# Performance work log

Measured on AMD Instinct MI355X. Metric: run time of the kernel, lower is better.

The kernel has to match this reference:

```python
import jax, jax.numpy as jnp
import numpy as np

B, N, D = 8, 1024, 768
H = 12
HD = D // H  # 64
SCALE = HD ** -0.5


def setup_inputs() -> dict:
    key = jax.random.key(0)
    k1, k2, k3 = jax.random.split(key, 3)
    x = jax.random.normal(k1, (B, N, D), dtype=jnp.float32)
    qkv_w = jax.random.normal(k2, (3 * D, D), dtype=jnp.float32) * 0.02
    proj_w = jax.random.normal(k3, (D, D), dtype=jnp.float32) * 0.02
    proj_b = jnp.zeros((D,), dtype=jnp.float32)
    return {"x": x, "qkv_w": qkv_w, "proj_w": proj_w, "proj_b": proj_b}


def reference(x, qkv_w, proj_w, proj_b):
    # qkv projection: [B,N,3D] -> [3,B,H,N,HD]
    qkv = jnp.einsum('bnd,ed->bne', x, qkv_w)
    qkv = qkv.reshape(B, N, 3, H, HD).transpose(2, 0, 3, 1, 4)
    q, k, v = qkv[0], qkv[1], qkv[2]
    # scaled dot-product attention
    attn = jnp.einsum('bhqd,bhkd->bhqk', q * SCALE, k)
    attn = jax.nn.softmax(attn, axis=-1)
    out = jnp.einsum('bhqk,bhkd->bhqd', attn, v)
    out = out.transpose(0, 2, 1, 3).reshape(B, N, D)
    # output projection
    return jnp.einsum('bnd,ed->bne', out, proj_w) + proj_b
```

## Files before the change

kernel.cpp:

```cpp
#include <hip/hip_runtime.h>

typedef unsigned short ushort;
typedef __attribute__((ext_vector_type(4)))  float  f32x4;
typedef __attribute__((ext_vector_type(16))) float  f32x16;
typedef __attribute__((ext_vector_type(8)))  short  s16x8;
typedef __attribute__((ext_vector_type(4)))  ushort u16x4;
typedef __attribute__((ext_vector_type(4)))  unsigned u32x4;

#define MFMA16(a, b, c) __builtin_amdgcn_mfma_f32_16x16x32_bf16((a), (b), (c), 0, 0, 0)
#define MFMA32(a, b, c) __builtin_amdgcn_mfma_f32_32x32x16_bf16((a), (b), (c), 0, 0, 0)

__device__ __forceinline__ ushort f2bf(float f) {
    unsigned u = __builtin_bit_cast(unsigned, f);
    u = (u + 0x7FFF + ((u >> 16) & 1)) >> 16;
    return (ushort)u;
}

__device__ __forceinline__ unsigned cvtpk_bf16(float lo, float hi) {
    unsigned r;
    asm("v_cvt_pk_bf16_f32 %0, %1, %2" : "=v"(r) : "v"(lo), "v"(hi));
    return r;
}
__device__ __forceinline__ void plswap(unsigned& a, unsigned& b) {
    asm volatile("v_permlane32_swap_b32 %0, %1" : "+v"(a), "+v"(b));
}
__device__ __forceinline__ float pairmax(float x) {
    unsigned a = __builtin_bit_cast(unsigned, x), b;
    asm("v_mov_b32 %0, %1" : "=v"(b) : "v"(a));
    plswap(a, b);
    return fmaxf(__builtin_bit_cast(float, a), __builtin_bit_cast(float, b));
}
__device__ __forceinline__ float pairsum(float x) {
    unsigned a = __builtin_bit_cast(unsigned, x), b;
    asm("v_mov_b32 %0, %1" : "=v"(b) : "v"(a));
    plswap(a, b);
    return __builtin_bit_cast(float, a) + __builtin_bit_cast(float, b);
}
__device__ __forceinline__ float fast_exp2(float x) {
    float r;
    asm("v_exp_f32 %0, %1" : "=v"(r) : "v"(x));
    return r;
}

__device__ __forceinline__ void gload_lds16(const ushort* g, ushort* l) {
    __builtin_amdgcn_global_load_lds(
        (const __attribute__((address_space(1))) void*)g,
        (__attribute__((address_space(3))) void*)l, 16, 0, 0);
}

__global__ __launch_bounds__(256) void cvt_all(
    const float* __restrict__ x, const float* __restrict__ wq,
    const float* __restrict__ wp, ushort* __restrict__ out,
    int n4x, int n4q, int n4p)
{
    int i = blockIdx.x * blockDim.x + threadIdx.x;
    const int stride = gridDim.x * blockDim.x;
    const int total = n4x + n4q + n4p;
    for (; i < total; i += stride) {
        float4 v;
        if (i < n4x)            v = ((const float4*)x)[i];
        else if (i < n4x + n4q) v = ((const float4*)wq)[i - n4x];
        else                    v = ((const float4*)wp)[i - n4x - n4q];
        u16x4 o;
        o[0] = f2bf(v.x); o[1] = f2bf(v.y); o[2] = f2bf(v.z); o[3] = f2bf(v.w);
        ((u16x4*)out)[i] = o;
    }
}

__device__ __forceinline__ void gemm128_mainloop(
    const ushort* __restrict__ A, const ushort* __restrict__ B, int K,
    int row0, int col0, ushort* As, ushort* Bs, f32x4 acc[4][4])
{
    const int t  = threadIdx.x;
    const int l  = t & 63;
    const int w  = t >> 6;
    const int lr = l & 15, lg = l >> 4;
    const int wm = w >> 1, wn = w & 1;

#pragma unroll
    for (int m = 0; m < 4; m++)
#pragma unroll
        for (int n = 0; n < 4; n++) acc[m][n] = (f32x4){0.f, 0.f, 0.f, 0.f};

    const int slot = (t & 3) ^ ((t >> 3) & 3);
    const ushort* ga0 = A + (row0 + (t >> 2)) * K + slot * 8;
    const ushort* gb0 = B + (col0 + (t >> 2)) * K + slot * 8;
    const int rowsz = 64 * K;
    ushort* la0 = As + t * 8;
    ushort* lb0 = Bs + t * 8;

    auto STAGE = [&](int kt, int buf) {
        const int k0  = kt * 32;
        const int off = buf * 4096;
        gload_lds16(ga0 + k0,         la0 + off);
        gload_lds16(ga0 + rowsz + k0, la0 + off + 2048);
        gload_lds16(gb0 + k0,         lb0 + off);
        gload_lds16(gb0 + rowsz + k0, lb0 + off + 2048);
    };
    const int sx = (lg ^ ((lr >> 1) & 3)) * 8;
    auto COMPUTE = [&](int buf) {
        const ushort* Ab = As + buf * 4096;
        const ushort* Bb = Bs + buf * 4096;
        s16x8 af[4], bfr[4];
#pragma unroll
        for (int m = 0; m < 4; m++)
            af[m] = *(const s16x8*)&Ab[(wm * 64 + m * 16 + lr) * 32 + sx];
#pragma unroll
        for (int n = 0; n < 4; n++)
            bfr[n] = *(const s16x8*)&Bb[(wn * 64 + n * 16 + lr) * 32 + sx];
        __builtin_amdgcn_s_setprio(1);
#pragma unroll
        for (int m = 0; m < 4; m++)
#pragma unroll
            for (int n = 0; n < 4; n++)
                acc[m][n] = MFMA16(af[m], bfr[n], acc[m][n]);
        __builtin_amdgcn_s_setprio(0);
    };

    const int nt = K >> 5;
    STAGE(0, 0);
    STAGE(1, 1);
    asm volatile("s_waitcnt vmcnt(4)" ::: "memory");
    __builtin_amdgcn_s_barrier();

#define GSTEP(IT, CBUF, SBUF)                                          \
    {                                                                  \
        const int sk = (IT) + 2;                                       \
        const bool st = sk < nt;                                       \
        if (st) STAGE(sk, SBUF);                                       \
        COMPUTE(CBUF);                                                 \
        if (st) { asm volatile("s_waitcnt vmcnt(4)" ::: "memory"); }   \
        else    { asm volatile("s_waitcnt vmcnt(0)" ::: "memory"); }   \
        __builtin_amdgcn_s_barrier();                                  \
    }

    for (int base = 0; base < nt; base += 3) {
        GSTEP(base,     0, 2);
        GSTEP(base + 1, 1, 0);
        GSTEP(base + 2, 2, 1);
    }
#undef GSTEP
}

__global__ __launch_bounds__(256) void qkv_gemm(
    const ushort* __restrict__ X, const ushort* __restrict__ W,
    ushort* __restrict__ qb, ushort* __restrict__ kb, ushort* __restrict__ vb)
{
    __shared__ __align__(16) ushort As[3 * 128 * 32];
    __shared__ __align__(16) ushort Bs[3 * 128 * 32];
    f32x4 acc[4][4];
    const int br = blockIdx.x, bc = blockIdx.y;
    gemm128_mainloop(X, W, 768, br * 128, bc * 128, As, Bs, acc);

    const int t = threadIdx.x, l = t & 63, w = t >> 6;
    const int lr = l & 15, lg = l >> 4, wm = w >> 1, wn = w & 1;
    const int p = (bc * 128) / 768;
    const int mrow0 = br * 128 + wm * 64 + lg * 4;
    const int ecolB = bc * 128 + wn * 64 + lr;
    const float QSCALE = 0.125f * 1.44269504088896f;

#pragma unroll
    for (int n = 0; n < 4; n++) {
        const int e   = ecolB + n * 16;
        const int rem = e - p * 768;
        const int h   = rem >> 6;
        const int hd  = rem & 63;
#pragma unroll
        for (int m = 0; m < 4; m++) {
            const int mr = mrow0 + m * 16;
            const int b  = mr >> 10;
            const int nn = mr & 1023;
            const f32x4 v = acc[m][n];
            const int bh = b * 12 + h;
            if (p == 0) {
                ushort* dst = qb + (bh * 1024 + nn) * 64 + hd;
#pragma unroll
                for (int r = 0; r < 4; r++) dst[r * 64] = f2bf(v[r] * QSCALE);
            } else if (p == 1) {
                ushort* dst = kb + (bh * 1024 + nn) * 64 + hd;
#pragma unroll
                for (int r = 0; r < 4; r++) dst[r * 64] = f2bf(v[r]);
            } else {
                u16x4 pk;
                pk[0] = f2bf(v[0]); pk[1] = f2bf(v[1]);
                pk[2] = f2bf(v[2]); pk[3] = f2bf(v[3]);
                *(u16x4*)(vb + (bh * 64 + hd) * 1024 + nn) = pk;
            }
        }
    }
}

__global__ __launch_bounds__(256) void attn_kernel(
    const ushort* __restrict__ qb, const ushort* __restrict__ kb,
    const ushort* __restrict__ vb, ushort* __restrict__ ao)
{
    __shared__ __align__(16) ushort KV[3][4096];
    const int bh = blockIdx.x, qt = blockIdx.y;
    const int b = bh / 12, h = bh - b * 12;
    const int t = threadIdx.x, l = t & 63, w = t >> 6;
    const int lq = l & 31, hi = l >> 5;
    const int qr0 = qt * 128 + w * 32;

    const int l3 = l >> 3, l7 = l & 7;
    const int ku = w * 8 + l3;
    const int pfv = l7 ^ l3;
    const char* ksrc = (const char*)kb + (size_t)(bh * 1024 + ku) * 128
                     + ((l7 ^ l3) << 4);
    const char* vsrc = (const char*)vb + (size_t)(bh * 64 + ku + 32 * ((pfv >> 2) & 1)) * 2048
                     + ((pfv & 3) << 4);
    ushort* kdst = &KV[0][0]    + t * 8;
    ushort* vdst = &KV[0][2048] + t * 8;

    auto STAGE = [&](int kt, int buf) {
        gload_lds16((const ushort*)(ksrc + kt * 32 * 128), kdst + buf * 4096);
        gload_lds16((const ushort*)(vsrc + kt * 32 * 2),   vdst + buf * 4096);
    };

    const ushort* qlane = qb + (bh * 1024 + qr0 + lq) * 64 + hi * 8;
    s16x8 qf[4];
#pragma unroll
    for (int s = 0; s < 4; s++) qf[s] = *(const s16x8*)(qlane + s * 16);

    float m = -__builtin_inff();
    float lsum = 0.f;
    f32x16 o0 = {}, o1 = {};

    STAGE(0, 0);
    STAGE(1, 1);
    asm volatile("s_waitcnt vmcnt(2)" ::: "memory");
    __builtin_amdgcn_s_barrier();

    const int fx = (lq & 7) << 4;
    int cur = 0;
    for (int it = 0; it < 32; ++it) {
        const bool st = it < 30;
        if (st) {
            int sb = cur + 2; if (sb >= 3) sb -= 3;
            STAGE(it + 2, sb);
        }
        const char* Kb = (const char*)&KV[cur][0];
        const char* Vb = (const char*)&KV[cur][2048];

        s16x8 kf[4];
#pragma unroll
        for (int s = 0; s < 4; s++)
            kf[s] = *(const s16x8*)(Kb + lq * 128 + ((hi * 16 + s * 32) ^ fx));

        f32x16 sa = {};
        __builtin_amdgcn_s_setprio(1);
#pragma unroll
        for (int s = 0; s < 4; s++) sa = MFMA32(kf[s], qf[s], sa);
        __builtin_amdgcn_s_setprio(0);

        float g0 = fmaxf(fmaxf(sa[0],  sa[1]),  sa[2]);
        float g1 = fmaxf(fmaxf(sa[3],  sa[4]),  sa[5]);
        float g2 = fmaxf(fmaxf(sa[6],  sa[7]),  sa[8]);
        float g3 = fmaxf(fmaxf(sa[9],  sa[10]), sa[11]);
        float g4 = fmaxf(fmaxf(sa[12], sa[13]), sa[14]);
        float h0 = fmaxf(fmaxf(g0, g1), g2);
        float h1 = fmaxf(fmaxf(g3, g4), sa[15]);
        const float mx = pairmax(fmaxf(h0, h1));

        if (!__all(mx <= m + 8.f)) {
            const float mn = fmaxf(m, mx);
            const float fac = fast_exp2(m - mn);
            m = mn;
            lsum *= fac;
#pragma unroll
            for (int r = 0; r < 16; r++) { o0[r] *= fac; o1[r] *= fac; }
        }

        float p[16];
#pragma unroll
        for (int r = 0; r < 16; r++) p[r] = fast_exp2(sa[r] - m);
        float ts[8];
#pragma unroll
        for (int r = 0; r < 8; r++) ts[r] = p[r] + p[r + 8];
#pragma unroll
        for (int s = 4; s; s >>= 1)
#pragma unroll
            for (int r = 0; r < s; r++) ts[r] += ts[r + s];
        lsum += pairsum(ts[0]);

        s16x8 pfr[2];
#pragma unroll
        for (int slot = 0; slot < 2; slot++) {
            const int r0 = slot * 8;
            unsigned a0 = cvtpk_bf16(p[r0 + 0], p[r0 + 1]);
            unsigned a1 = cvtpk_bf16(p[r0 + 4], p[r0 + 5]);
            plswap(a0, a1);
            unsigned b0 = cvtpk_bf16(p[r0 + 2], p[r0 + 3]);
            unsigned b1 = cvtpk_bf16(p[r0 + 6], p[r0 + 7]);
            plswap(b0, b1);
            const u32x4 u = {a0, b0, a1, b1};
            pfr[slot] = __builtin_bit_cast(s16x8, u);
        }

        s16x8 vf[2][2];
#pragma unroll
        for (int half = 0; half < 2; half++)
#pragma unroll
            for (int s = 0; s < 2; s++)
                vf[half][s] = *(const s16x8*)(Vb + lq * 128 + ((half * 64 + hi * 16 + s * 32) ^ fx));
        __builtin_amdgcn_s_setprio(1);
        o0 = MFMA32(vf[0][0], pfr[0], o0);
        o1 = MFMA32(vf[1][0], pfr[0], o1);
        o0 = MFMA32(vf[0][1], pfr[1], o0);
        o1 = MFMA32(vf[1][1], pfr[1], o1);
        __builtin_amdgcn_s_setprio(0);

        if (st) { asm volatile("s_waitcnt vmcnt(2)" ::: "memory"); }
        else    { asm volatile("s_waitcnt vmcnt(0)" ::: "memory"); }
        __builtin_amdgcn_s_barrier();
        cur = (cur == 2) ? 0 : cur + 1;
    }

    const float inv = 1.f / lsum;
    ushort* op = ao + (b * 1024 + qr0 + lq) * 768 + h * 64 + 4 * hi;
#pragma unroll
    for (int i = 0; i < 4; i++) {
        u16x4 pk0, pk1;
#pragma unroll
        for (int j = 0; j < 4; j++) {
            pk0[j] = f2bf(o0[4 * i + j] * inv);
            pk1[j] = f2bf(o1[4 * i + j] * inv);
        }
        *(u16x4*)(op + 8 * i)      = pk0;
        *(u16x4*)(op + 32 + 8 * i) = pk1;
    }
}

__global__ __launch_bounds__(256) void proj_gemm(
    const ushort* __restrict__ A, const ushort* __restrict__ W,
    const float* __restrict__ bias, float* __restrict__ out)
{
    __shared__ __align__(16) ushort As[3 * 64 * 32];
    __shared__ __align__(16) ushort Bs[3 * 128 * 32];
    const int t = threadIdx.x, l = t & 63, w = t >> 6;
    const int lr = l & 15, lg = l >> 4;
    const int wm = w >> 1, wn = w & 1;
    const int br = blockIdx.x, bc = blockIdx.y;

    f32x4 acc[2][4];
#pragma unroll
    for (int m = 0; m < 2; m++)
#pragma unroll
        for (int n = 0; n < 4; n++) acc[m][n] = (f32x4){0.f, 0.f, 0.f, 0.f};

    const int slot = (t & 3) ^ ((t >> 3) & 3);
    const ushort* ga0 = A + (br * 64 + (t >> 2)) * 768 + slot * 8;
    const ushort* gb0 = W + (bc * 128 + (t >> 2)) * 768 + slot * 8;
    ushort* la0 = As + t * 8;
    ushort* lb0 = Bs + t * 8;

    auto STAGE = [&](int kt, int buf) {
        const int k0 = kt * 32;
        gload_lds16(ga0 + k0,            la0 + buf * 2048);
        gload_lds16(gb0 + k0,            lb0 + buf * 4096);
        gload_lds16(gb0 + 64 * 768 + k0, lb0 + buf * 4096 + 2048);
    };
    const int sx = (lg ^ ((lr >> 1) & 3)) * 8;
    auto COMPUTE = [&](int buf) {
        const ushort* Ab = As + buf * 2048;
        const ushort* Bb = Bs + buf * 4096;
        s16x8 af[2], bfr[4];
#pragma unroll
        for (int m = 0; m < 2; m++)
            af[m] = *(const s16x8*)&Ab[(wm * 32 + m * 16 + lr) * 32 + sx];
#pragma unroll
        for (int n = 0; n < 4; n++)
            bfr[n] = *(const s16x8*)&Bb[(wn * 64 + n * 16 + lr) * 32 + sx];
        __builtin_amdgcn_s_setprio(1);
#pragma unroll
        for (int m = 0; m < 2; m++)
#pragma unroll
            for (int n = 0; n < 4; n++)
                acc[m][n] = MFMA16(af[m], bfr[n], acc[m][n]);
        __builtin_amdgcn_s_setprio(0);
    };

    const int nt = 24;
    STAGE(0, 0);
    STAGE(1, 1);
    asm volatile("s_waitcnt vmcnt(3)" ::: "memory");
    __builtin_amdgcn_s_barrier();

#define GSTEP(IT, CBUF, SBUF)                                          \
    {                                                                  \
        const int sk = (IT) + 2;                                       \
        const bool st = sk < nt;                                       \
        if (st) STAGE(sk, SBUF);                                       \
        COMPUTE(CBUF);                                                 \
        if (st) { asm volatile("s_waitcnt vmcnt(3)" ::: "memory"); }   \
        else    { asm volatile("s_waitcnt vmcnt(0)" ::: "memory"); }   \
        __builtin_amdgcn_s_barrier();                                  \
    }

    for (int base = 0; base < nt; base += 3) {
        GSTEP(base,     0, 2);
        GSTEP(base + 1, 1, 0);
        GSTEP(base + 2, 2, 1);
    }
#undef GSTEP

    const int mrow0 = br * 64 + wm * 32 + lg * 4;
    const int ecolB = bc * 128 + wn * 64 + lr;
#pragma unroll
    for (int n = 0; n < 4; n++) {
        const int e = ecolB + n * 16;
        const float bv = bias[e];
#pragma unroll
        for (int m = 0; m < 2; m++) {
            const int mr = mrow0 + m * 16;
#pragma unroll
            for (int r = 0; r < 4; r++)
                out[(mr + r) * 768 + e] = acc[m][n][r] + bv;
        }
    }
}

extern "C" void kernel_launch(void* const* d_in, const int* in_sizes, int n_in,
                              void* d_out, int out_size, void* d_ws, size_t ws_size,
                              hipStream_t stream)
{
    const float* x  = (const float*)d_in[0];
    const float* wq = (const float*)d_in[1];
    const float* wp = (const float*)d_in[2];
    const float* pb = (const float*)d_in[3];
    float* out = (float*)d_out;

    const int NX = 8 * 1024 * 768;
    const int NQ = 2304 * 768;
    const int NP = 768 * 768;
    const int SEG = 8 * 12 * 1024 * 64;

    ushort* xb  = (ushort*)d_ws;
    ushort* wqb = xb + NX;
    ushort* wpb = wqb + NQ;
    ushort* qb  = wpb + NP;
    ushort* kb  = qb + SEG;
    ushort* vb  = kb + SEG;
    ushort* ao  = xb;

    cvt_all<<<2048, 256, 0, stream>>>(x, wq, wp, xb, NX / 4, NQ / 4, NP / 4);

    qkv_gemm  <<<dim3(64, 18), 256, 0, stream>>>(xb, wqb, qb, kb, vb);
    attn_kernel<<<dim3(96, 8), 256, 0, stream>>>(qb, kb, vb, ao);
    proj_gemm <<<dim3(128, 6), 256, 0, stream>>>(ao, wpb, pb, out);
}
```

Measured before the change: 119.5 us.

## Split attention KV range across wave pairs and merge partial softmax states

Each attention block now handles 64 query rows instead of 128. Two waves share each 32-row strip, and each wave processes half of the key/value sequence, so the grid doubles to 96x16. The partial max, sum and output from the two halves are merged through LDS at the end. The staging changes from a 3-deep ring to double buffering, with __syncthreads in place of the finer vmcnt waits. The aim is more blocks and shorter serial loops per wave, at the cost of a merge step, a full barrier every iteration, and less prefetch depth.

```diff
diff --git a/kernel.cpp b/kernel.cpp
--- a/kernel.cpp
+++ b/kernel.cpp
@@ -194,26 +194,31 @@
     const ushort* __restrict__ qb, const ushort* __restrict__ kb,
     const ushort* __restrict__ vb, ushort* __restrict__ ao)
 {
-    __shared__ __align__(16) ushort KV[3][4096];
+    __shared__ __align__(16) ushort KV[2][8192];
     const int bh = blockIdx.x, qt = blockIdx.y;
     const int b = bh / 12, h = bh - b * 12;
     const int t = threadIdx.x, l = t & 63, w = t >> 6;
     const int lq = l & 31, hi = l >> 5;
-    const int qr0 = qt * 128 + w * 32;
-
-    const int l3 = l >> 3, l7 = l & 7;
-    const int ku = w * 8 + l3;
-    const int pfv = l7 ^ l3;
-    const char* ksrc = (const char*)kb + (size_t)(bh * 1024 + ku) * 128
-                     + ((l7 ^ l3) << 4);
-    const char* vsrc = (const char*)vb + (size_t)(bh * 64 + ku + 32 * ((pfv >> 2) & 1)) * 2048
+    const int strip = w & 1, half = w >> 1;
+    const int qr0 = qt * 64 + strip * 32;
+
+    const int u   = t >> 3;
+    const int pfv = (t & 7) ^ (u & 7);
+    const char* ksrc = (const char*)kb + (size_t)(bh * 1024 + u) * 128 + (pfv << 4);
+    const char* vsrc = (const char*)vb
+                     + (size_t)(bh * 64 + u + 32 * ((pfv >> 2) & 1)) * 2048
                      + ((pfv & 3) << 4);
-    ushort* kdst = &KV[0][0]    + t * 8;
-    ushort* vdst = &KV[0][2048] + t * 8;
+    ushort* kd0 = &KV[0][0]    + t * 8;
+    ushort* vd0 = &KV[0][2048] + t * 8;
+    ushort* kd1 = &KV[0][4096] + t * 8;
+    ushort* vd1 = &KV[0][6144] + t * 8;
 
     auto STAGE = [&](int kt, int buf) {
-        gload_lds16((const ushort*)(ksrc + kt * 32 * 128), kdst + buf * 4096);
-        gload_lds16((const ushort*)(vsrc + kt * 32 * 2),   vdst + buf * 4096);
+        const int bo = buf * 8192;
+        gload_lds16((const ushort*)(ksrc + kt * 4096),           kd0 + bo);
+        gload_lds16((const ushort*)(vsrc + kt * 64),             vd0 + bo);
+        gload_lds16((const ushort*)(ksrc + 65536 + kt * 4096),   kd1 + bo);
+        gload_lds16((const ushort*)(vsrc + 1024 + kt * 64),      vd1 + bo);
     };
 
     const ushort* qlane = qb + (bh * 1024 + qr0 + lq) * 64 + hi * 8;
@@ -226,20 +231,15 @@
     f32x16 o0 = {}, o1 = {};
 
     STAGE(0, 0);
-    STAGE(1, 1);
-    asm volatile("s_waitcnt vmcnt(2)" ::: "memory");
-    __builtin_amdgcn_s_barrier();
+    __syncthreads();
 
     const int fx = (lq & 7) << 4;
-    int cur = 0;
-    for (int it = 0; it < 32; ++it) {
-        const bool st = it < 30;
-        if (st) {
-            int sb = cur + 2; if (sb >= 3) sb -= 3;
-            STAGE(it + 2, sb);
-        }
-        const char* Kb = (const char*)&KV[cur][0];
-        const char* Vb = (const char*)&KV[cur][2048];
+    const int hoff = half * 8192;
+    for (int it = 0; it < 16; ++it) {
+        const int cur = it & 1;
+        if (it < 15) STAGE(it + 1, cur ^ 1);
+        const char* Kb = (const char*)&KV[cur][0] + hoff;
+        const char* Vb = Kb + 4096;
 
         s16x8 kf[4];
 #pragma unroll
@@ -292,16 +292,16 @@
             unsigned b0 = cvtpk_bf16(p[r0 + 2], p[r0 + 3]);
             unsigned b1 = cvtpk_bf16(p[r0 + 6], p[r0 + 7]);
             plswap(b0, b1);
-            const u32x4 u = {a0, b0, a1, b1};
-            pfr[slot] = __builtin_bit_cast(s16x8, u);
+            const u32x4 uu = {a0, b0, a1, b1};
+            pfr[slot] = __builtin_bit_cast(s16x8, uu);
         }
 
         s16x8 vf[2][2];
 #pragma unroll
-        for (int half = 0; half < 2; half++)
+        for (int hd = 0; hd < 2; hd++)
 #pragma unroll
             for (int s = 0; s < 2; s++)
-                vf[half][s] = *(const s16x8*)(Vb + lq * 128 + ((half * 64 + hi * 16 + s * 32) ^ fx));
+                vf[hd][s] = *(const s16x8*)(Vb + lq * 128 + ((hd * 64 + hi * 16 + s * 32) ^ fx));
         __builtin_amdgcn_s_setprio(1);
         o0 = MFMA32(vf[0][0], pfr[0], o0);
         o1 = MFMA32(vf[1][0], pfr[0], o1);
@@ -309,24 +309,45 @@
         o1 = MFMA32(vf[1][1], pfr[1], o1);
         __builtin_amdgcn_s_setprio(0);
 
-        if (st) { asm volatile("s_waitcnt vmcnt(2)" ::: "memory"); }
-        else    { asm volatile("s_waitcnt vmcnt(0)" ::: "memory"); }
-        __builtin_amdgcn_s_barrier();
-        cur = (cur == 2) ? 0 : cur + 1;
-    }
-
-    const float inv = 1.f / lsum;
-    ushort* op = ao + (b * 1024 + qr0 + lq) * 768 + h * 64 + 4 * hi;
-#pragma unroll
-    for (int i = 0; i < 4; i++) {
-        u16x4 pk0, pk1;
-#pragma unroll
-        for (int j = 0; j < 4; j++) {
-            pk0[j] = f2bf(o0[4 * i + j] * inv);
-            pk1[j] = f2bf(o1[4 * i + j] * inv);
-        }
-        *(u16x4*)(op + 8 * i)      = pk0;
-        *(u16x4*)(op + 32 + 8 * i) = pk1;
+        __syncthreads();
+    }
+
+    float* ex = (float*)&KV[0][0];
+    float* sb = ex + strip * 2176;
+    __syncthreads();
+    if (half == 1) {
+        sb[l] = m;
+        sb[64 + l] = lsum;
+#pragma unroll
+        for (int r = 0; r < 16; r++) sb[128  + r * 64 + l] = o0[r];
+#pragma unroll
+        for (int r = 0; r < 16; r++) sb[1152 + r * 64 + l] = o1[r];
+    }
+    __syncthreads();
+    if (half == 0) {
+        const float mb = sb[l], lb = sb[64 + l];
+        const float mm = fmaxf(m, mb);
+        const float fa = fast_exp2(m - mm);
+        const float fb = fast_exp2(mb - mm);
+        const float lt = lsum * fa + lb * fb;
+#pragma unroll
+        for (int r = 0; r < 16; r++) {
+            o0[r] = o0[r] * fa + sb[128  + r * 64 + l] * fb;
+            o1[r] = o1[r] * fa + sb[1152 + r * 64 + l] * fb;
+        }
+        const float inv = 1.f / lt;
+        ushort* op = ao + (b * 1024 + qr0 + lq) * 768 + h * 64 + 4 * hi;
+#pragma unroll
+        for (int i = 0; i < 4; i++) {
+            u16x4 pk0, pk1;
+#pragma unroll
+            for (int j = 0; j < 4; j++) {
+                pk0[j] = f2bf(o0[4 * i + j] * inv);
+                pk1[j] = f2bf(o1[4 * i + j] * inv);
+            }
+            *(u16x4*)(op + 8 * i)      = pk0;
+            *(u16x4*)(op + 32 + 8 * i) = pk1;
+        }
     }
 }
 
@@ -445,6 +466,6 @@
     cvt_all<<<2048, 256, 0, stream>>>(x, wq, wp, xb, NX / 4, NQ / 4, NP / 4);
 
     qkv_gemm  <<<dim3(64, 18), 256, 0, stream>>>(xb, wqb, qb, kb, vb);
-    attn_kernel<<<dim3(96, 8), 256, 0, stream>>>(qb, kb, vb, ao);
+    attn_kernel<<<dim3(96, 16), 256, 0, stream>>>(qb, kb, vb, ao);
     proj_gemm <<<dim3(128, 6), 256, 0, stream>>>(ao, wpb, pb, out);
 }
```

Result: no change. 120.5 us (+0.8%).

## Replace triple-buffered K/V LDS pipeline with double buffering

Applied to the files above, without the earlier changes.

The attention kernel's K/V staging goes from three LDS buffers with prefetch distance two to two buffers with prefetch distance one. The explicit vmcnt waits are replaced by __syncthreads. This cuts LDS use per block from 24 KB to 16 KB, which may allow more blocks per CU. In exchange, less global-load latency is hidden, and __syncthreads likely waits for all outstanding loads every iteration.

```diff
diff --git a/kernel.cpp b/kernel.cpp
--- a/kernel.cpp
+++ b/kernel.cpp
@@ -194,7 +194,7 @@
     const ushort* __restrict__ qb, const ushort* __restrict__ kb,
     const ushort* __restrict__ vb, ushort* __restrict__ ao)
 {
-    __shared__ __align__(16) ushort KV[3][4096];
+    __shared__ __align__(16) ushort KV[2][4096];
     const int bh = blockIdx.x, qt = blockIdx.y;
     const int b = bh / 12, h = bh - b * 12;
     const int t = threadIdx.x, l = t & 63, w = t >> 6;
@@ -208,13 +208,8 @@
                      + ((l7 ^ l3) << 4);
     const char* vsrc = (const char*)vb + (size_t)(bh * 64 + ku + 32 * ((pfv >> 2) & 1)) * 2048
                      + ((pfv & 3) << 4);
-    ushort* kdst = &KV[0][0]    + t * 8;
-    ushort* vdst = &KV[0][2048] + t * 8;
-
-    auto STAGE = [&](int kt, int buf) {
-        gload_lds16((const ushort*)(ksrc + kt * 32 * 128), kdst + buf * 4096);
-        gload_lds16((const ushort*)(vsrc + kt * 32 * 2),   vdst + buf * 4096);
-    };
+    ushort* kdst = &KV[0][0]    + w * 512 + l * 8;
+    ushort* vdst = &KV[0][2048] + w * 512 + l * 8;
 
     const ushort* qlane = qb + (bh * 1024 + qr0 + lq) * 64 + hi * 8;
     s16x8 qf[4];
@@ -225,18 +220,17 @@
     float lsum = 0.f;
     f32x16 o0 = {}, o1 = {};
 
-    STAGE(0, 0);
-    STAGE(1, 1);
-    asm volatile("s_waitcnt vmcnt(2)" ::: "memory");
-    __builtin_amdgcn_s_barrier();
+    gload_lds16((const ushort*)ksrc, kdst);
+    gload_lds16((const ushort*)vsrc, vdst);
+    __syncthreads();
 
     const int fx = (lq & 7) << 4;
-    int cur = 0;
     for (int it = 0; it < 32; ++it) {
-        const bool st = it < 30;
-        if (st) {
-            int sb = cur + 2; if (sb >= 3) sb -= 3;
-            STAGE(it + 2, sb);
+        const int cur = it & 1;
+        if (it < 31) {
+            const int kvn = (it + 1) * 32;
+            gload_lds16((const ushort*)(ksrc + kvn * 128), kdst + (cur ^ 1) * 4096);
+            gload_lds16((const ushort*)(vsrc + kvn * 2),   vdst + (cur ^ 1) * 4096);
         }
         const char* Kb = (const char*)&KV[cur][0];
         const char* Vb = (const char*)&KV[cur][2048];
@@ -309,10 +303,7 @@
         o1 = MFMA32(vf[1][1], pfr[1], o1);
         __builtin_amdgcn_s_setprio(0);
 
-        if (st) { asm volatile("s_waitcnt vmcnt(2)" ::: "memory"); }
-        else    { asm volatile("s_waitcnt vmcnt(0)" ::: "memory"); }
-        __builtin_amdgcn_s_barrier();
-        cur = (cur == 2) ? 0 : cur + 1;
+        __syncthreads();
     }
 
     const float inv = 1.f / lsum;
```

Measured after the change: 116.2 us. -2.8%, faster.
